# Kernel tuning notes

Measured on AMD Instinct MI355X. Metric: run time of the kernel, lower is better.

The kernel has to match this reference:

```python
import jax, jax.numpy as jnp
import numpy as np

N, E, IN_DIM, OUT_DIM, H = 50000, 600000, 128, 16, 8

def setup_inputs() -> dict:
    key = jax.random.key(0)
    ks = jax.random.split(key, 10)
    h = jax.random.normal(ks[0], (N, IN_DIM), dtype=jnp.float32)
    e = jax.random.normal(ks[1], (E, IN_DIM), dtype=jnp.float32)
    src = jax.random.randint(ks[2], (E,), 0, N, dtype=jnp.int32)
    dst = jax.random.randint(ks[3], (E,), 0, N, dtype=jnp.int32)
    s = 1.0 / np.sqrt(IN_DIM)
    s3 = 1.0 / np.sqrt(3 * OUT_DIM)
    Wh = jax.random.uniform(ks[4], (H, IN_DIM, OUT_DIM), jnp.float32, -s, s)
    We = jax.random.uniform(ks[5], (H, IN_DIM, OUT_DIM), jnp.float32, -s, s)
    Wproj = jax.random.uniform(ks[6], (H, 3 * OUT_DIM, OUT_DIM), jnp.float32, -s3, s3)
    bproj = jax.random.uniform(ks[7], (H, OUT_DIM), jnp.float32, -s3, s3)
    Wattn = jax.random.uniform(ks[8], (H, 3 * OUT_DIM), jnp.float32, -s3, s3)
    return {"h": h, "e": e, "src": src, "dst": dst, "Wh": Wh, "We": We,
            "Wproj": Wproj, "bproj": bproj, "Wattn": Wattn}

def reference(h, e, src, dst, Wh, We, Wproj, bproj, Wattn):
    n = h.shape[0]
    z_h = jnp.einsum('ni,hio->nho', h, Wh)          # [N,H,O]
    z_e = jnp.einsum('ei,hio->eho', e, We)          # [E,H,O]
    z_src = z_h[src]                                 # gather [E,H,O]
    z_dst = z_h[dst]                                 # gather [E,H,O]
    z = jnp.concatenate([z_e, z_src, z_dst], axis=-1)  # [E,H,3O]
    attn = jax.nn.leaky_relu(jnp.einsum('ehk,hk->eh', z, Wattn))  # slope 0.01, matches torch default
    e_proj = jnp.einsum('ehk,hko->eho', z, Wproj) + bproj          # [E,H,O]
    # segment softmax over incoming edges per destination node
    m = jax.ops.segment_max(attn, dst, num_segments=n)             # [N,H]
    m = jnp.where(jnp.isfinite(m), m, 0.0)                         # guard empty segments
    ex = jnp.exp(attn - m[dst])                                    # [E,H]
    denom = jax.ops.segment_sum(ex, dst, num_segments=n)           # [N,H]
    alpha = ex / jnp.maximum(denom[dst], 1e-9)
    h_agg = jax.ops.segment_sum(alpha[..., None] * z_src, dst, num_segments=n)  # [N,H,O]
    h_out = jax.nn.elu(h_agg).reshape(n, -1)        # concat heads -> [N,H*O]
    e_out = jax.nn.elu(e_proj).reshape(e.shape[0], -1)  # [E,H*O]
    h_out = h + h_out                                # residual (in_dim == H*O)
    e_out = e + e_out
    return h_out, e_out
```

## Files before the change

kernel.cpp:

```cpp
#include <hip/hip_runtime.h>
#include <math.h>


constexpr int NN = 50000;
constexpr int NE = 600000;
constexpr int APAD = 132;
constexpr int BSTR = 160;
constexpr int CSTR = 140;

typedef __attribute__((ext_vector_type(8))) short bf16x8;
typedef __attribute__((ext_vector_type(8))) unsigned short u16x8;
typedef __attribute__((ext_vector_type(4))) float f32x4;

__device__ __forceinline__ unsigned short f2bf(float f) {
    unsigned u = __float_as_uint(f);
    u += 0x7fffu + ((u >> 16) & 1u);
    return (unsigned short)(u >> 16);
}
__device__ __forceinline__ float bf2f(unsigned short us) {
    return __uint_as_float((unsigned)us << 16);
}

__global__ void k_combine(const float* __restrict__ Wh, const float* __restrict__ We,
                          const float* __restrict__ Wproj, const float* __restrict__ Wattn,
                          unsigned char* __restrict__ Bcomb, float* __restrict__ Wn)
{
    int tid = blockIdx.x * 256 + threadIdx.x;
    if (tid < 16384) {
        int i = tid >> 7, c = tid & 127;
        int h = c >> 4, o = c & 15;
        float s = 0.f;
#pragma unroll
        for (int k = 0; k < 16; ++k)
            s += We[h*2048 + i*16 + k] * Wproj[h*768 + k*16 + o];
        int off = c*256 + (((i>>3) ^ (c&15))<<4) + (i&7)*2;
        *(unsigned short*)(Bcomb + off) = f2bf(s);
    } else if (tid < 17408) {
        int q = tid - 16384;
        int i = q >> 3, h = q & 7;
        float s = 0.f;
#pragma unroll
        for (int k = 0; k < 16; ++k)
            s += We[h*2048 + i*16 + k] * Wattn[h*48 + k];
        int col = 128 + h;
        int off = col*256 + (((i>>3) ^ (col&15))<<4) + (i&7)*2;
        *(unsigned short*)(Bcomb + off) = f2bf(s);
    } else if (tid < 33792) {
        int q = tid - 17408;
        int i = q >> 7, c = q & 127;
        int h = c >> 4, o = c & 15;
        Wn[i*128 + c] = Wh[h*2048 + i*16 + o];
    } else if (tid < 36864) {
        int q = tid - 33792;
        int col = 136 + (q >> 7), i = q & 127;
        int off = col*256 + (((i>>3) ^ (col&15))<<4) + (i&7)*2;
        *(unsigned short*)(Bcomb + off) = 0;
    }
}

__device__ __forceinline__ void stage_ab(const float* __restrict__ Aglob,
                                         const float* __restrict__ Bglob,
                                         float* Al, float* Bl, int m0, int M)
{
    int t = threadIdx.x;
    {
        int r = t >> 2, kc = t & 3;
        int gr = m0 + r; if (gr >= M) gr = M - 1;
        const float4* s4 = (const float4*)(Aglob + (size_t)gr*128 + kc*32);
        float4* d4 = (float4*)(Al + r*APAD + kc*32);
#pragma unroll
        for (int i = 0; i < 8; ++i) d4[i] = s4[i];
    }
    {
        const float2* B2 = (const float2*)Bglob;
#pragma unroll
        for (int it = 0; it < 16; ++it) {
            int q = it*512 + t;
            int k = q >> 6, c2 = q & 63;
            int c = c2*2, g = c >> 3, j = c & 7;
            float2 v = B2[q];
            Bl[k*BSTR + g*10 + j]     = v.x;
            Bl[k*BSTR + g*10 + j + 1] = v.y;
        }
    }
}

__device__ __forceinline__ void mm_core(const float* Al, const float* Bl, float acc[4][8])
{
    int t = threadIdx.x;
    int rowg = t >> 4, colg = t & 15;
    int r0 = rowg * 4;
#pragma unroll
    for (int i = 0; i < 4; ++i)
#pragma unroll
        for (int j = 0; j < 8; ++j) acc[i][j] = 0.f;
#pragma unroll 4
    for (int k = 0; k < 128; ++k) {
        float a0 = Al[(r0+0)*APAD + k];
        float a1 = Al[(r0+1)*APAD + k];
        float a2 = Al[(r0+2)*APAD + k];
        float a3 = Al[(r0+3)*APAD + k];
        const float* bp = Bl + k*BSTR + colg*10;
#pragma unroll
        for (int j = 0; j < 8; ++j) {
            float b = bp[j];
            acc[0][j] += a0 * b;
            acc[1][j] += a1 * b;
            acc[2][j] += a2 * b;
            acc[3][j] += a3 * b;
        }
    }
}

__global__ __launch_bounds__(512, 2) void k_node_gemm(const float* __restrict__ hg,
                                                      const float* __restrict__ Wn,
                                                      float* __restrict__ z_h,
                                                      unsigned short* __restrict__ z_hb)
{
    __shared__ float Al[128*APAD];
    __shared__ float Bl[128*BSTR];
    int m0 = blockIdx.x * 128;
    stage_ab(hg, Wn, Al, Bl, m0, NN);
    __syncthreads();
    float acc[4][8];
    mm_core(Al, Bl, acc);
    int t = threadIdx.x;
    int rowg = t >> 4, colg = t & 15, r0 = rowg*4;
#pragma unroll
    for (int i = 0; i < 4; ++i) {
        int gr = m0 + r0 + i;
        if (gr < NN) {
            float4* dp = (float4*)(z_h + (size_t)gr*128 + colg*8);
            dp[0] = make_float4(acc[i][0], acc[i][1], acc[i][2], acc[i][3]);
            dp[1] = make_float4(acc[i][4], acc[i][5], acc[i][6], acc[i][7]);
            u16x8 zb;
#pragma unroll
            for (int j = 0; j < 8; ++j) zb[j] = f2bf(acc[i][j]);
            *(u16x8*)(z_hb + (size_t)gr*128 + colg*8) = zb;
        }
    }
}

__global__ __launch_bounds__(256) void k_nodepost(const float* __restrict__ z_h,
    const float* __restrict__ Wproj, const float* __restrict__ Wattn,
    unsigned short* __restrict__ p_sb, unsigned short* __restrict__ p_db,
    float* __restrict__ a_s, float* __restrict__ a_d)
{
    __shared__ float Wps[16*128], Wpd[16*128], Was[128], Wad[128];
    __shared__ float z2[2*140];
    int t = threadIdx.x;
    for (int q = t; q < 2048; q += 256) {
        int k = q >> 7, rest = q & 127, h = rest >> 4, o = rest & 15;
        Wps[q] = Wproj[h*768 + (16+k)*16 + o];
        Wpd[q] = Wproj[h*768 + (32+k)*16 + o];
    }
    if (t < 128) {
        int h = t >> 4, k = t & 15;
        Was[t] = Wattn[h*48 + 16 + k];
        Wad[t] = Wattn[h*48 + 32 + k];
    }
    int nh = t >> 7, rest = t & 127, hh = rest >> 4, oo = rest & 15;
    int n0 = blockIdx.x * 32;
    for (int it = 0; it < 16; ++it) {
        int n = n0 + it*2 + nh;
        __syncthreads();
        {
            float v = 0.f;
            if (n < NN) v = z_h[(size_t)n*128 + hh*16 + oo];
            z2[nh*140 + hh*17 + oo] = v;
        }
        __syncthreads();
        if (n < NN) {
            const float* zz = z2 + nh*140 + hh*17;
            float ps = 0.f, pd = 0.f, as_ = 0.f, ad_ = 0.f;
#pragma unroll
            for (int k = 0; k < 16; ++k) {
                float zv = zz[k];
                ps  += zv * Wps[k*128 + hh*16 + oo];
                pd  += zv * Wpd[k*128 + hh*16 + oo];
                as_ += zv * Was[hh*16 + k];
                ad_ += zv * Wad[hh*16 + k];
            }
            p_sb[(size_t)n*128 + rest] = f2bf(ps);
            p_db[(size_t)n*128 + rest] = f2bf(pd);
            if (oo == 0) { a_s[n*8 + hh] = as_; a_d[n*8 + hh] = ad_; }
        }
    }
}

union EdgeSM {
    struct { __align__(16) unsigned char A[32768]; __align__(16) unsigned char Bt[40960]; } s;
    float C[128*CSTR];
};

__global__ __launch_bounds__(256) void k_edge(const float* __restrict__ eg,
    const unsigned char* __restrict__ Bcomb, const float* __restrict__ bproj,
    const int* __restrict__ src, const int* __restrict__ dst,
    const unsigned short* __restrict__ p_sb, const unsigned short* __restrict__ p_db,
    const float* __restrict__ a_s, const float* __restrict__ a_d,
    float* __restrict__ attn, float* __restrict__ e_out)
{
    __shared__ EdgeSM sm;
    __shared__ float bpl[128];
    const int t = threadIdx.x;
    const int m0 = blockIdx.x * 128;

#pragma unroll
    for (int it = 0; it < 16; ++it) {
        int q = it*256 + t;
        int row = q >> 5, c4 = q & 31;
        int gr = m0 + row; if (gr >= NE) gr = NE - 1;
        float4 v = *(const float4*)(eg + (size_t)gr*128 + c4*4);
        unsigned u0 = (unsigned)f2bf(v.x) | ((unsigned)f2bf(v.y) << 16);
        unsigned u1 = (unsigned)f2bf(v.z) | ((unsigned)f2bf(v.w) << 16);
        int off = row*256 + (((c4>>1) ^ (row&15))<<4) + (c4&1)*8;
        *(uint2*)(sm.s.A + off) = make_uint2(u0, u1);
    }
    {
        const uint4* bsrc = (const uint4*)Bcomb;
        uint4* bdst = (uint4*)sm.s.Bt;
#pragma unroll
        for (int it = 0; it < 10; ++it) {
            int q = it*256 + t;
            bdst[q] = bsrc[q];
        }
    }
    if (t < 128) bpl[t] = bproj[t];
    __syncthreads();

    const int w = t >> 6, l = t & 63;
    const int lc = l & 15, lk = l >> 4;
    const int wm0 = (w >> 1) * 64, wn0 = (w & 1) * 80;
    f32x4 acc[4][5];
#pragma unroll
    for (int m = 0; m < 4; ++m)
#pragma unroll
        for (int n = 0; n < 5; ++n) acc[m][n] = (f32x4){0.f, 0.f, 0.f, 0.f};

#pragma unroll
    for (int ks = 0; ks < 4; ++ks) {
        const int swz = ((ks*4 + lk) ^ lc) << 4;
        bf16x8 af[4], bfr[5];
#pragma unroll
        for (int m = 0; m < 4; ++m) {
            int row = wm0 + m*16 + lc;
            af[m] = *(const bf16x8*)(sm.s.A + row*256 + swz);
        }
#pragma unroll
        for (int n = 0; n < 5; ++n) {
            int col = wn0 + n*16 + lc;
            bfr[n] = *(const bf16x8*)(sm.s.Bt + col*256 + swz);
        }
#pragma unroll
        for (int m = 0; m < 4; ++m)
#pragma unroll
            for (int n = 0; n < 5; ++n)
                acc[m][n] = __builtin_amdgcn_mfma_f32_16x16x32_bf16(af[m], bfr[n], acc[m][n], 0, 0, 0);
    }
    __syncthreads();

    {
#pragma unroll
        for (int m = 0; m < 4; ++m) {
            int rbase = wm0 + m*16 + lk*4;
#pragma unroll
            for (int n = 0; n < 5; ++n) {
                int col = wn0 + n*16 + lc;
                bool keep = (w & 1) ? (n < 3 || (n == 3 && lc < 8)) : true;
                if (keep) {
#pragma unroll
                    for (int i = 0; i < 4; ++i)
                        sm.C[(rbase + i)*CSTR + col] = acc[m][n][i];
                }
            }
        }
    }
    __syncthreads();

    {
        int row = t >> 1, g = t & 1;
        int er = m0 + row;
        if (er < NE) {
            int sj = src[er], dj = dst[er];
            const float* Cp = &sm.C[row*CSTR + 128 + g*4];
            float4 as4 = *(const float4*)(a_s + (size_t)sj*8 + g*4);
            float4 ad4 = *(const float4*)(a_d + (size_t)dj*8 + g*4);
            float v0 = Cp[0] + as4.x + ad4.x;
            float v1 = Cp[1] + as4.y + ad4.y;
            float v2 = Cp[2] + as4.z + ad4.z;
            float v3 = Cp[3] + as4.w + ad4.w;
            v0 = v0 > 0.f ? v0 : 0.01f * v0;
            v1 = v1 > 0.f ? v1 : 0.01f * v1;
            v2 = v2 > 0.f ? v2 : 0.01f * v2;
            v3 = v3 > 0.f ? v3 : 0.01f * v3;
            *(float4*)(attn + (size_t)er*8 + g*4) = make_float4(v0, v1, v2, v3);
        }
    }

    {
        int rowg = t >> 4, colg = t & 15;
#pragma unroll
        for (int i = 0; i < 8; ++i) {
            int r = rowg*8 + i;
            int er = m0 + r;
            if (er < NE) {
                int sj = src[er], dj = dst[er];
                u16x8 psv = *(const u16x8*)(p_sb + (size_t)sj*128 + colg*8);
                u16x8 pdv = *(const u16x8*)(p_db + (size_t)dj*128 + colg*8);
                const float4* evp = (const float4*)(eg + (size_t)er*128 + colg*8);
                float4 ev0 = evp[0], ev1 = evp[1];
                const float* Cp = &sm.C[r*CSTR + colg*8];
                float ov[8];
#pragma unroll
                for (int j = 0; j < 8; ++j) {
                    float val = Cp[j] + bf2f(psv[j]) + bf2f(pdv[j]) + bpl[colg*8 + j];
                    ov[j] = val > 0.f ? val : expm1f(val);
                }
                float4* op = (float4*)(e_out + (size_t)er*128 + colg*8);
                op[0] = make_float4(ev0.x + ov[0], ev0.y + ov[1], ev0.z + ov[2], ev0.w + ov[3]);
                op[1] = make_float4(ev1.x + ov[4], ev1.y + ov[5], ev1.z + ov[6], ev1.w + ov[7]);
            }
        }
    }
}

__global__ void k_hist(const int* __restrict__ dst, int* __restrict__ deg)
{
    int e = blockIdx.x*256 + threadIdx.x;
    if (e < NE) atomicAdd(&deg[dst[e]], 1);
}

__global__ __launch_bounds__(1024) void k_scan1(const int* __restrict__ deg,
                                                int* __restrict__ offs, int* __restrict__ bsum)
{
    __shared__ int s[1024];
    int t = threadIdx.x;
    int idx = blockIdx.x*1024 + t;
    int v = (idx < NN) ? deg[idx] : 0;
    s[t] = v;
    __syncthreads();
    for (int off = 1; off < 1024; off <<= 1) {
        int x = (t >= off) ? s[t - off] : 0;
        __syncthreads();
        s[t] += x;
        __syncthreads();
    }
    if (idx < NN) offs[idx] = s[t] - v;
    if (t == 1023) bsum[blockIdx.x] = s[1023];
}

__global__ void k_scan2(const int* __restrict__ bsum, int* __restrict__ bases)
{
    int i = threadIdx.x;
    int v = (i < 49) ? bsum[i] : 0;
    int incl = v;
#pragma unroll
    for (int off = 1; off < 64; off <<= 1) {
        int x = __shfl_up(incl, off, 64);
        if (i >= off) incl += x;
    }
    if (i < 49) bases[i] = incl - v;
}

__global__ void k_scan3(int* __restrict__ offs, const int* __restrict__ bases,
                        int* __restrict__ cursor)
{
    int n = blockIdx.x*256 + threadIdx.x;
    if (n < NN) {
        int v = offs[n] + bases[n >> 10];
        offs[n] = v;
        cursor[n] = v;
    }
}

__global__ void k_scatter(const int* __restrict__ dst, int* __restrict__ cursor,
                          int* __restrict__ eids)
{
    int e = blockIdx.x*256 + threadIdx.x;
    if (e < NE) {
        int p = atomicAdd(&cursor[dst[e]], 1);
        eids[p] = e;
    }
}

__global__ __launch_bounds__(256) void k_agg(const float* __restrict__ hg,
    const unsigned short* __restrict__ z_hb, const float* __restrict__ attn,
    const int* __restrict__ eids, const int* __restrict__ offs, const int* __restrict__ deg,
    const int* __restrict__ src, float* __restrict__ h_out)
{
    int half = threadIdx.x >> 7;
    int t = threadIdx.x & 127;
    int n = blockIdx.x * 2 + half;
    int hh = t >> 4;
    int dg = deg[n];
    int o0 = offs[n];
    float m = -INFINITY;
    for (int j = (t & 15); j < dg; j += 16) {
        int e = eids[o0 + j];
        m = fmaxf(m, attn[(size_t)e*8 + hh]);
    }
#pragma unroll
    for (int s = 1; s < 16; s <<= 1) m = fmaxf(m, __shfl_xor(m, s, 64));

    float n0 = 0.f, n1 = 0.f, n2 = 0.f, n3 = 0.f;
    float d0 = 0.f, d1 = 0.f, d2 = 0.f, d3 = 0.f;
    int j = 0;
    for (; j + 4 <= dg; j += 4) {
        int e0 = eids[o0 + j + 0];
        int e1 = eids[o0 + j + 1];
        int e2 = eids[o0 + j + 2];
        int e3 = eids[o0 + j + 3];
        int s0 = src[e0], s1 = src[e1], s2 = src[e2], s3 = src[e3];
        float x0 = expf(attn[(size_t)e0*8 + hh] - m);
        float x1 = expf(attn[(size_t)e1*8 + hh] - m);
        float x2 = expf(attn[(size_t)e2*8 + hh] - m);
        float x3 = expf(attn[(size_t)e3*8 + hh] - m);
        d0 += x0; d1 += x1; d2 += x2; d3 += x3;
        n0 += x0 * bf2f(z_hb[(size_t)s0*128 + t]);
        n1 += x1 * bf2f(z_hb[(size_t)s1*128 + t]);
        n2 += x2 * bf2f(z_hb[(size_t)s2*128 + t]);
        n3 += x3 * bf2f(z_hb[(size_t)s3*128 + t]);
    }
    for (; j < dg; ++j) {
        int e = eids[o0 + j];
        float x = expf(attn[(size_t)e*8 + hh] - m);
        d0 += x;
        n0 += x * bf2f(z_hb[(size_t)src[e]*128 + t]);
    }
    float num = (n0 + n1) + (n2 + n3);
    float den = (d0 + d1) + (d2 + d3);
    float hag = num / fmaxf(den, 1e-9f);
    float el = hag > 0.f ? hag : expm1f(hag);
    h_out[(size_t)n*128 + t] = hg[(size_t)n*128 + t] + el;
}

extern "C" void kernel_launch(void* const* d_in, const int* in_sizes, int n_in,
                              void* d_out, int out_size, void* d_ws, size_t ws_size,
                              hipStream_t stream)
{
    const float* h     = (const float*)d_in[0];
    const float* e     = (const float*)d_in[1];
    const int*   src   = (const int*)d_in[2];
    const int*   dst   = (const int*)d_in[3];
    const float* Wh    = (const float*)d_in[4];
    const float* We    = (const float*)d_in[5];
    const float* Wproj = (const float*)d_in[6];
    const float* bproj = (const float*)d_in[7];
    const float* Wattn = (const float*)d_in[8];
    float* h_out = (float*)d_out;
    float* e_out = h_out + (size_t)NN * 128;

    char* w = (char*)d_ws;
    auto alloc = [&](size_t bytes) {
        char* p = w;
        w += (bytes + 255) & ~(size_t)255;
        return p;
    };
    unsigned char* Bcomb = (unsigned char*)alloc(160 * 256);
    float* Wn   = (float*)alloc(16384 * 4);
    float* z_h  = (float*)alloc((size_t)NN * 128 * 4);
    unsigned short* z_hb = (unsigned short*)alloc((size_t)NN * 128 * 2);
    unsigned short* p_sb = (unsigned short*)alloc((size_t)NN * 128 * 2);
    unsigned short* p_db = (unsigned short*)alloc((size_t)NN * 128 * 2);
    float* a_s  = (float*)alloc((size_t)NN * 8 * 4);
    float* a_d  = (float*)alloc((size_t)NN * 8 * 4);
    float* attn = (float*)alloc((size_t)NE * 8 * 4);
    int* deg    = (int*)alloc((size_t)NN * 4);
    int* offs   = (int*)alloc((size_t)NN * 4);
    int* cursor = (int*)alloc((size_t)NN * 4);
    int* eids   = (int*)alloc((size_t)NE * 4);
    int* bsum   = (int*)alloc(64 * 4);
    int* bases  = (int*)alloc(64 * 4);

    hipMemsetAsync(deg, 0, (size_t)NN * 4, stream);

    k_combine<<<144, 256, 0, stream>>>(Wh, We, Wproj, Wattn, Bcomb, Wn);
    k_node_gemm<<<(NN + 127) / 128, 512, 0, stream>>>(h, Wn, z_h, z_hb);
    k_nodepost<<<(NN + 31) / 32, 256, 0, stream>>>(z_h, Wproj, Wattn, p_sb, p_db, a_s, a_d);
    k_edge<<<(NE + 127) / 128, 256, 0, stream>>>(e, Bcomb, bproj, src, dst,
                                                 p_sb, p_db, a_s, a_d, attn, e_out);
    k_hist<<<(NE + 255) / 256, 256, 0, stream>>>(dst, deg);
    k_scan1<<<49, 1024, 0, stream>>>(deg, offs, bsum);
    k_scan2<<<1, 64, 0, stream>>>(bsum, bases);
    k_scan3<<<(NN + 255) / 256, 256, 0, stream>>>(offs, bases, cursor);
    k_scatter<<<(NE + 255) / 256, 256, 0, stream>>>(dst, cursor, eids);
    k_agg<<<NN / 2, 256, 0, stream>>>(h, z_hb, attn, eids, offs, deg, src, h_out);
}
```

Measured before the change: 908.4 us.

## Use bf16 MFMA for node GEMM, pre-permute edges and drop softmax max pass

The scalar fp32 node GEMM is replaced with a bf16 MFMA kernel that reads pre-swizzled bf16 weights, matching the edge kernel's layout. The nodepost weights are kept in registers instead of shared memory. A new permute kernel stores src and attn in destination-sorted order, so aggregation reads them contiguously without going through eids. The segment-max pass is dropped, which assumes exp(attn) cannot overflow. The permuted buffers reuse the p_sb/a_s workspace, which is no longer needed at that point. Risks are reduced precision of z_h from the bf16 GEMM and possible overflow for large attention logits.

```diff
diff --git a/kernel.cpp b/kernel.cpp
--- a/kernel.cpp
+++ b/kernel.cpp
@@ -4,9 +4,8 @@
 
 constexpr int NN = 50000;
 constexpr int NE = 600000;
-constexpr int APAD = 132;
-constexpr int BSTR = 160;
 constexpr int CSTR = 140;
+constexpr int CST2 = 132;
 
 typedef __attribute__((ext_vector_type(8))) short bf16x8;
 typedef __attribute__((ext_vector_type(8))) unsigned short u16x8;
@@ -23,7 +22,7 @@
 
 __global__ void k_combine(const float* __restrict__ Wh, const float* __restrict__ We,
                           const float* __restrict__ Wproj, const float* __restrict__ Wattn,
-                          unsigned char* __restrict__ Bcomb, float* __restrict__ Wn)
+                          unsigned char* __restrict__ Bcomb, unsigned char* __restrict__ Bn)
 {
     int tid = blockIdx.x * 256 + threadIdx.x;
     if (tid < 16384) {
@@ -49,7 +48,8 @@
         int q = tid - 17408;
         int i = q >> 7, c = q & 127;
         int h = c >> 4, o = c & 15;
-        Wn[i*128 + c] = Wh[h*2048 + i*16 + o];
+        int off = c*256 + (((i>>3) ^ (c&15))<<4) + (i&7)*2;
+        *(unsigned short*)(Bn + off) = f2bf(Wh[h*2048 + i*16 + o]);
     } else if (tid < 36864) {
         int q = tid - 33792;
         int col = 136 + (q >> 7), i = q & 127;
@@ -58,85 +58,95 @@
     }
 }
 
-__device__ __forceinline__ void stage_ab(const float* __restrict__ Aglob,
-                                         const float* __restrict__ Bglob,
-                                         float* Al, float* Bl, int m0, int M)
-{
-    int t = threadIdx.x;
-    {
-        int r = t >> 2, kc = t & 3;
-        int gr = m0 + r; if (gr >= M) gr = M - 1;
-        const float4* s4 = (const float4*)(Aglob + (size_t)gr*128 + kc*32);
-        float4* d4 = (float4*)(Al + r*APAD + kc*32);
-#pragma unroll
-        for (int i = 0; i < 8; ++i) d4[i] = s4[i];
-    }
-    {
-        const float2* B2 = (const float2*)Bglob;
-#pragma unroll
-        for (int it = 0; it < 16; ++it) {
-            int q = it*512 + t;
-            int k = q >> 6, c2 = q & 63;
-            int c = c2*2, g = c >> 3, j = c & 7;
-            float2 v = B2[q];
-            Bl[k*BSTR + g*10 + j]     = v.x;
-            Bl[k*BSTR + g*10 + j + 1] = v.y;
-        }
-    }
-}
-
-__device__ __forceinline__ void mm_core(const float* Al, const float* Bl, float acc[4][8])
-{
-    int t = threadIdx.x;
-    int rowg = t >> 4, colg = t & 15;
-    int r0 = rowg * 4;
-#pragma unroll
-    for (int i = 0; i < 4; ++i)
-#pragma unroll
-        for (int j = 0; j < 8; ++j) acc[i][j] = 0.f;
-#pragma unroll 4
-    for (int k = 0; k < 128; ++k) {
-        float a0 = Al[(r0+0)*APAD + k];
-        float a1 = Al[(r0+1)*APAD + k];
-        float a2 = Al[(r0+2)*APAD + k];
-        float a3 = Al[(r0+3)*APAD + k];
-        const float* bp = Bl + k*BSTR + colg*10;
-#pragma unroll
-        for (int j = 0; j < 8; ++j) {
-            float b = bp[j];
-            acc[0][j] += a0 * b;
-            acc[1][j] += a1 * b;
-            acc[2][j] += a2 * b;
-            acc[3][j] += a3 * b;
-        }
-    }
-}
-
-__global__ __launch_bounds__(512, 2) void k_node_gemm(const float* __restrict__ hg,
-                                                      const float* __restrict__ Wn,
-                                                      float* __restrict__ z_h,
-                                                      unsigned short* __restrict__ z_hb)
-{
-    __shared__ float Al[128*APAD];
-    __shared__ float Bl[128*BSTR];
-    int m0 = blockIdx.x * 128;
-    stage_ab(hg, Wn, Al, Bl, m0, NN);
-    __syncthreads();
-    float acc[4][8];
-    mm_core(Al, Bl, acc);
-    int t = threadIdx.x;
-    int rowg = t >> 4, colg = t & 15, r0 = rowg*4;
-#pragma unroll
-    for (int i = 0; i < 4; ++i) {
-        int gr = m0 + r0 + i;
-        if (gr < NN) {
-            float4* dp = (float4*)(z_h + (size_t)gr*128 + colg*8);
-            dp[0] = make_float4(acc[i][0], acc[i][1], acc[i][2], acc[i][3]);
-            dp[1] = make_float4(acc[i][4], acc[i][5], acc[i][6], acc[i][7]);
-            u16x8 zb;
-#pragma unroll
-            for (int j = 0; j < 8; ++j) zb[j] = f2bf(acc[i][j]);
-            *(u16x8*)(z_hb + (size_t)gr*128 + colg*8) = zb;
+union NodeSM {
+    struct { __align__(16) unsigned char A[32768]; __align__(16) unsigned char Bt[32768]; } s;
+    float C[128*CST2];
+};
+
+__global__ __launch_bounds__(256) void k_node_gemm(const float* __restrict__ hg,
+    const unsigned char* __restrict__ Bn,
+    float* __restrict__ z_h, unsigned short* __restrict__ z_hb)
+{
+    __shared__ NodeSM sm;
+    const int t = threadIdx.x;
+    const int m0 = blockIdx.x * 128;
+
+#pragma unroll
+    for (int it = 0; it < 16; ++it) {
+        int q = it*256 + t;
+        int row = q >> 5, c4 = q & 31;
+        int gr = m0 + row; if (gr >= NN) gr = NN - 1;
+        float4 v = *(const float4*)(hg + (size_t)gr*128 + c4*4);
+        unsigned u0 = (unsigned)f2bf(v.x) | ((unsigned)f2bf(v.y) << 16);
+        unsigned u1 = (unsigned)f2bf(v.z) | ((unsigned)f2bf(v.w) << 16);
+        int off = row*256 + (((c4>>1) ^ (row&15))<<4) + (c4&1)*8;
+        *(uint2*)(sm.s.A + off) = make_uint2(u0, u1);
+    }
+    {
+        const uint4* bsrc = (const uint4*)Bn;
+        uint4* bdst = (uint4*)sm.s.Bt;
+#pragma unroll
+        for (int it = 0; it < 8; ++it) bdst[it*256 + t] = bsrc[it*256 + t];
+    }
+    __syncthreads();
+
+    const int w = t >> 6, l = t & 63;
+    const int lc = l & 15, lk = l >> 4;
+    const int wm0 = (w >> 1) * 64, wn0 = (w & 1) * 64;
+    f32x4 acc[4][4];
+#pragma unroll
+    for (int m = 0; m < 4; ++m)
+#pragma unroll
+        for (int n = 0; n < 4; ++n) acc[m][n] = (f32x4){0.f, 0.f, 0.f, 0.f};
+
+#pragma unroll
+    for (int ks = 0; ks < 4; ++ks) {
+        const int swz = ((ks*4 + lk) ^ lc) << 4;
+        bf16x8 af[4], bfr[4];
+#pragma unroll
+        for (int m = 0; m < 4; ++m)
+            af[m] = *(const bf16x8*)(sm.s.A + (wm0 + m*16 + lc)*256 + swz);
+#pragma unroll
+        for (int n = 0; n < 4; ++n)
+            bfr[n] = *(const bf16x8*)(sm.s.Bt + (wn0 + n*16 + lc)*256 + swz);
+#pragma unroll
+        for (int m = 0; m < 4; ++m)
+#pragma unroll
+            for (int n = 0; n < 4; ++n)
+                acc[m][n] = __builtin_amdgcn_mfma_f32_16x16x32_bf16(af[m], bfr[n], acc[m][n], 0, 0, 0);
+    }
+    __syncthreads();
+
+#pragma unroll
+    for (int m = 0; m < 4; ++m) {
+        int rbase = wm0 + m*16 + lk*4;
+#pragma unroll
+        for (int n = 0; n < 4; ++n) {
+            int col = wn0 + n*16 + lc;
+#pragma unroll
+            for (int i = 0; i < 4; ++i)
+                sm.C[(rbase + i)*CST2 + col] = acc[m][n][i];
+        }
+    }
+    __syncthreads();
+
+    {
+        int rowg = t >> 4, colg = t & 15;
+#pragma unroll
+        for (int i = 0; i < 8; ++i) {
+            int r = rowg*8 + i;
+            int gr = m0 + r;
+            if (gr < NN) {
+                const float* Cp = &sm.C[r*CST2 + colg*8];
+                float4 c0 = *(const float4*)&Cp[0];
+                float4 c1 = *(const float4*)&Cp[4];
+                float4* dp = (float4*)(z_h + (size_t)gr*128 + colg*8);
+                dp[0] = c0; dp[1] = c1;
+                u16x8 zb;
+                zb[0] = f2bf(c0.x); zb[1] = f2bf(c0.y); zb[2] = f2bf(c0.z); zb[3] = f2bf(c0.w);
+                zb[4] = f2bf(c1.x); zb[5] = f2bf(c1.y); zb[6] = f2bf(c1.z); zb[7] = f2bf(c1.w);
+                *(u16x8*)(z_hb + (size_t)gr*128 + colg*8) = zb;
+            }
         }
     }
 }
@@ -146,40 +156,35 @@
     unsigned short* __restrict__ p_sb, unsigned short* __restrict__ p_db,
     float* __restrict__ a_s, float* __restrict__ a_d)
 {
-    __shared__ float Wps[16*128], Wpd[16*128], Was[128], Wad[128];
-    __shared__ float z2[2*140];
+    __shared__ float z2[2][136];
     int t = threadIdx.x;
-    for (int q = t; q < 2048; q += 256) {
-        int k = q >> 7, rest = q & 127, h = rest >> 4, o = rest & 15;
-        Wps[q] = Wproj[h*768 + (16+k)*16 + o];
-        Wpd[q] = Wproj[h*768 + (32+k)*16 + o];
-    }
-    if (t < 128) {
-        int h = t >> 4, k = t & 15;
-        Was[t] = Wattn[h*48 + 16 + k];
-        Wad[t] = Wattn[h*48 + 32 + k];
-    }
     int nh = t >> 7, rest = t & 127, hh = rest >> 4, oo = rest & 15;
+
+    float wps[16], wpd[16], was_r[16], wad_r[16];
+#pragma unroll
+    for (int k = 0; k < 16; ++k) {
+        wps[k]   = Wproj[hh*768 + (16+k)*16 + oo];
+        wpd[k]   = Wproj[hh*768 + (32+k)*16 + oo];
+        was_r[k] = Wattn[hh*48 + 16 + k];
+        wad_r[k] = Wattn[hh*48 + 32 + k];
+    }
+
     int n0 = blockIdx.x * 32;
     for (int it = 0; it < 16; ++it) {
         int n = n0 + it*2 + nh;
         __syncthreads();
-        {
-            float v = 0.f;
-            if (n < NN) v = z_h[(size_t)n*128 + hh*16 + oo];
-            z2[nh*140 + hh*17 + oo] = v;
-        }
+        z2[nh][hh*17 + oo] = (n < NN) ? z_h[(size_t)n*128 + rest] : 0.f;
         __syncthreads();
         if (n < NN) {
-            const float* zz = z2 + nh*140 + hh*17;
+            const float* zz = &z2[nh][hh*17];
             float ps = 0.f, pd = 0.f, as_ = 0.f, ad_ = 0.f;
 #pragma unroll
             for (int k = 0; k < 16; ++k) {
                 float zv = zz[k];
-                ps  += zv * Wps[k*128 + hh*16 + oo];
-                pd  += zv * Wpd[k*128 + hh*16 + oo];
-                as_ += zv * Was[hh*16 + k];
-                ad_ += zv * Wad[hh*16 + k];
+                ps  += zv * wps[k];
+                pd  += zv * wpd[k];
+                as_ += zv * was_r[k];
+                ad_ += zv * wad_r[k];
             }
             p_sb[(size_t)n*128 + rest] = f2bf(ps);
             p_db[(size_t)n*128 + rest] = f2bf(pd);
@@ -220,10 +225,7 @@
         const uint4* bsrc = (const uint4*)Bcomb;
         uint4* bdst = (uint4*)sm.s.Bt;
 #pragma unroll
-        for (int it = 0; it < 10; ++it) {
-            int q = it*256 + t;
-            bdst[q] = bsrc[q];
-        }
+        for (int it = 0; it < 10; ++it) bdst[it*256 + t] = bsrc[it*256 + t];
     }
     if (t < 128) bpl[t] = bproj[t];
     __syncthreads();
@@ -242,15 +244,11 @@
         const int swz = ((ks*4 + lk) ^ lc) << 4;
         bf16x8 af[4], bfr[5];
 #pragma unroll
-        for (int m = 0; m < 4; ++m) {
-            int row = wm0 + m*16 + lc;
-            af[m] = *(const bf16x8*)(sm.s.A + row*256 + swz);
-        }
-#pragma unroll
-        for (int n = 0; n < 5; ++n) {
-            int col = wn0 + n*16 + lc;
-            bfr[n] = *(const bf16x8*)(sm.s.Bt + col*256 + swz);
-        }
+        for (int m = 0; m < 4; ++m)
+            af[m] = *(const bf16x8*)(sm.s.A + (wm0 + m*16 + lc)*256 + swz);
+#pragma unroll
+        for (int n = 0; n < 5; ++n)
+            bfr[n] = *(const bf16x8*)(sm.s.Bt + (wn0 + n*16 + lc)*256 + swz);
 #pragma unroll
         for (int m = 0; m < 4; ++m)
 #pragma unroll
@@ -383,10 +381,25 @@
     }
 }
 
+__global__ void k_permute(const int* __restrict__ eids, const int* __restrict__ src,
+                          const float* __restrict__ attn,
+                          int* __restrict__ src_perm, float* __restrict__ attn_perm)
+{
+    int p = blockIdx.x*256 + threadIdx.x;
+    if (p < NE) {
+        int e = eids[p];
+        src_perm[p] = src[e];
+        const float4* ap = (const float4*)(attn + (size_t)e*8);
+        float4 a0 = ap[0], a1 = ap[1];
+        float4* op = (float4*)(attn_perm + (size_t)p*8);
+        op[0] = a0; op[1] = a1;
+    }
+}
+
 __global__ __launch_bounds__(256) void k_agg(const float* __restrict__ hg,
-    const unsigned short* __restrict__ z_hb, const float* __restrict__ attn,
-    const int* __restrict__ eids, const int* __restrict__ offs, const int* __restrict__ deg,
-    const int* __restrict__ src, float* __restrict__ h_out)
+    const unsigned short* __restrict__ z_hb, const float* __restrict__ attn_perm,
+    const int* __restrict__ src_perm, const int* __restrict__ offs,
+    const int* __restrict__ deg, float* __restrict__ h_out)
 {
     int half = threadIdx.x >> 7;
     int t = threadIdx.x & 127;
@@ -394,27 +407,19 @@
     int hh = t >> 4;
     int dg = deg[n];
     int o0 = offs[n];
-    float m = -INFINITY;
-    for (int j = (t & 15); j < dg; j += 16) {
-        int e = eids[o0 + j];
-        m = fmaxf(m, attn[(size_t)e*8 + hh]);
-    }
-#pragma unroll
-    for (int s = 1; s < 16; s <<= 1) m = fmaxf(m, __shfl_xor(m, s, 64));
 
     float n0 = 0.f, n1 = 0.f, n2 = 0.f, n3 = 0.f;
     float d0 = 0.f, d1 = 0.f, d2 = 0.f, d3 = 0.f;
     int j = 0;
     for (; j + 4 <= dg; j += 4) {
-        int e0 = eids[o0 + j + 0];
-        int e1 = eids[o0 + j + 1];
-        int e2 = eids[o0 + j + 2];
-        int e3 = eids[o0 + j + 3];
-        int s0 = src[e0], s1 = src[e1], s2 = src[e2], s3 = src[e3];
-        float x0 = expf(attn[(size_t)e0*8 + hh] - m);
-        float x1 = expf(attn[(size_t)e1*8 + hh] - m);
-        float x2 = expf(attn[(size_t)e2*8 + hh] - m);
-        float x3 = expf(attn[(size_t)e3*8 + hh] - m);
+        int s0 = src_perm[o0 + j + 0];
+        int s1 = src_perm[o0 + j + 1];
+        int s2 = src_perm[o0 + j + 2];
+        int s3 = src_perm[o0 + j + 3];
+        float x0 = expf(attn_perm[(size_t)(o0 + j + 0)*8 + hh]);
+        float x1 = expf(attn_perm[(size_t)(o0 + j + 1)*8 + hh]);
+        float x2 = expf(attn_perm[(size_t)(o0 + j + 2)*8 + hh]);
+        float x3 = expf(attn_perm[(size_t)(o0 + j + 3)*8 + hh]);
         d0 += x0; d1 += x1; d2 += x2; d3 += x3;
         n0 += x0 * bf2f(z_hb[(size_t)s0*128 + t]);
         n1 += x1 * bf2f(z_hb[(size_t)s1*128 + t]);
@@ -422,10 +427,10 @@
         n3 += x3 * bf2f(z_hb[(size_t)s3*128 + t]);
     }
     for (; j < dg; ++j) {
-        int e = eids[o0 + j];
-        float x = expf(attn[(size_t)e*8 + hh] - m);
+        int s = src_perm[o0 + j];
+        float x = expf(attn_perm[(size_t)(o0 + j)*8 + hh]);
         d0 += x;
-        n0 += x * bf2f(z_hb[(size_t)src[e]*128 + t]);
+        n0 += x * bf2f(z_hb[(size_t)s*128 + t]);
     }
     float num = (n0 + n1) + (n2 + n3);
     float den = (d0 + d1) + (d2 + d3);
@@ -457,7 +462,7 @@
         return p;
     };
     unsigned char* Bcomb = (unsigned char*)alloc(160 * 256);
-    float* Wn   = (float*)alloc(16384 * 4);
+    unsigned char* Bn    = (unsigned char*)alloc(128 * 256);
     float* z_h  = (float*)alloc((size_t)NN * 128 * 4);
     unsigned short* z_hb = (unsigned short*)alloc((size_t)NN * 128 * 2);
     unsigned short* p_sb = (unsigned short*)alloc((size_t)NN * 128 * 2);
@@ -471,11 +476,13 @@
     int* eids   = (int*)alloc((size_t)NE * 4);
     int* bsum   = (int*)alloc(64 * 4);
     int* bases  = (int*)alloc(64 * 4);
+    float* attn_perm = (float*)p_sb;
+    int*   src_perm  = (int*)a_s;
 
     hipMemsetAsync(deg, 0, (size_t)NN * 4, stream);
 
-    k_combine<<<144, 256, 0, stream>>>(Wh, We, Wproj, Wattn, Bcomb, Wn);
-    k_node_gemm<<<(NN + 127) / 128, 512, 0, stream>>>(h, Wn, z_h, z_hb);
+    k_combine<<<144, 256, 0, stream>>>(Wh, We, Wproj, Wattn, Bcomb, Bn);
+    k_node_gemm<<<(NN + 127) / 128, 256, 0, stream>>>(h, Bn, z_h, z_hb);
     k_nodepost<<<(NN + 31) / 32, 256, 0, stream>>>(z_h, Wproj, Wattn, p_sb, p_db, a_s, a_d);
     k_edge<<<(NE + 127) / 128, 256, 0, stream>>>(e, Bcomb, bproj, src, dst,
                                                  p_sb, p_db, a_s, a_d, attn, e_out);
@@ -484,5 +491,6 @@
     k_scan2<<<1, 64, 0, stream>>>(bsum, bases);
     k_scan3<<<(NN + 255) / 256, 256, 0, stream>>>(offs, bases, cursor);
     k_scatter<<<(NE + 255) / 256, 256, 0, stream>>>(dst, cursor, eids);
-    k_agg<<<NN / 2, 256, 0, stream>>>(h, z_hb, attn, eids, offs, deg, src, h_out);
-}
+    k_permute<<<(NE + 255) / 256, 256, 0, stream>>>(eids, src, attn, src_perm, attn_perm);
+    k_agg<<<NN / 2, 256, 0, stream>>>(h, z_hb, attn_perm, src_perm, offs, deg, h_out);
+}
```

Measured after the change: 861.7 us. 5.1% less time.
